# Kernel tuning notes

Hardware: AMD Instinct MI355X
Metric: run time of the kernel (lower is better)

## Reference

```python
import jax, jax.numpy as jnp
import numpy as np

N, IN_DIM, OUT_DIM, H = 50000, 128, 128, 4
C = OUT_DIM // H  # 32, per-head channels
E = 1_600_000
NEG_SLOPE = 0.2
LN_EPS = 1e-5


def setup_inputs() -> dict:
    key = jax.random.key(0)
    ks = jax.random.split(key, 12)
    x = jax.random.normal(ks[0], (N, IN_DIM), dtype=jnp.float32)
    edge_index = jax.random.randint(ks[1], (2, E), 0, N, dtype=jnp.int64)
    edge_weight = jax.random.uniform(ks[2], (E,), dtype=jnp.float32)
    s = 1.0 / np.sqrt(IN_DIM)
    W = jax.random.normal(ks[3], (IN_DIM, H * C), dtype=jnp.float32) * s
    att_src = jax.random.normal(ks[4], (1, H, C), dtype=jnp.float32) * s
    att_dst = jax.random.normal(ks[5], (1, H, C), dtype=jnp.float32) * s
    W_edge = jax.random.normal(ks[6], (1, H * C), dtype=jnp.float32)
    att_edge = jax.random.normal(ks[7], (1, H, C), dtype=jnp.float32) * s
    bias = jnp.zeros((H * C,), dtype=jnp.float32)
    ln_gamma = jnp.ones((OUT_DIM,), dtype=jnp.float32)
    ln_beta = jnp.zeros((OUT_DIM,), dtype=jnp.float32)
    return {"x": x, "edge_index": edge_index, "edge_weight": edge_weight,
            "W": W, "att_src": att_src, "att_dst": att_dst,
            "W_edge": W_edge, "att_edge": att_edge, "bias": bias,
            "ln_gamma": ln_gamma, "ln_beta": ln_beta}


def _gat_forward(x, edge_index, edge_weight, W, att_src, att_dst, W_edge, att_edge, bias):
    # GATConv(in, C, heads=H, edge_dim=1), concat=True, add_self_loops=True (fill_value='mean')
    xp = (x @ W).reshape(N, H, C)                      # [N,H,C]
    a_src = jnp.sum(xp * att_src, axis=-1)             # [N,H]
    a_dst = jnp.sum(xp * att_dst, axis=-1)             # [N,H]

    # add self-loops; self-loop edge_attr = mean of existing edge_attr
    loop = jnp.arange(N, dtype=edge_index.dtype)
    src = jnp.concatenate([edge_index[0], loop])       # [E+N]
    dst = jnp.concatenate([edge_index[1], loop])
    ew = jnp.concatenate([edge_weight, jnp.full((N,), jnp.mean(edge_weight), edge_weight.dtype)])

    ea = (ew[:, None] @ W_edge).reshape(-1, H, C)      # [E+N,H,C]
    a_edge = jnp.sum(ea * att_edge, axis=-1)           # [E+N,H]

    logits = a_src[src] + a_dst[dst] + a_edge          # [E+N,H]
    logits = jax.nn.leaky_relu(logits, NEG_SLOPE)

    # segment softmax over destination-node neighborhoods
    m = jax.ops.segment_max(logits, dst, num_segments=N)     # [N,H]
    ex = jnp.exp(logits - m[dst])
    denom = jax.ops.segment_sum(ex, dst, num_segments=N)     # [N,H]
    attn = ex / (denom[dst] + 1e-16)                          # [E+N,H]

    msg = attn[:, :, None] * xp[src]                          # [E+N,H,C]
    out = jax.ops.segment_sum(msg, dst, num_segments=N)      # [N,H,C]
    return out.reshape(N, H * C) + bias


def reference(x, edge_index, edge_weight, W, att_src, att_dst, W_edge, att_edge, bias, ln_gamma, ln_beta):
    out = _gat_forward(x, edge_index, edge_weight, W, att_src, att_dst, W_edge, att_edge, bias)
    # LayerNorm
    mu = jnp.mean(out, axis=-1, keepdims=True)
    var = jnp.mean(jnp.square(out - mu), axis=-1, keepdims=True)
    out = (out - mu) / jnp.sqrt(var + LN_EPS) * ln_gamma + ln_beta
    # ELU (dropout is identity in eval)
    return jax.nn.elu(out)
```

## Files before the change

### kernel.cpp

```cpp
#include <hip/hip_runtime.h>
#include <hip/hip_fp16.h>
#include <cstddef>

#define N_NODES 50000
#define E_EDGES 1600000
#define NEG_SLOPE 0.2f
#define LN_EPS 1e-5f
#define LOG2E 1.4426950408889634f
#define PAD 96

#define NBK 196
#define BCAP 10240
#define PCH 4096
#define NCH 391
#define NGB 1563
#define TPB 256

#define OFF_SCAL    0u
#define OFF_BCUR    256u
#define OFF_EWPART  2048u
#define OFF_COUNTS  8192u
#define OFF_ASRC    208256u
#define OFF_ADST    1008256u
#define OFF_XPH     1808256u
#define OFF_PAIRS   14608256u
#define OFF_STAGE   33808256u

__device__ __forceinline__ float lrelu(float x) { return x > 0.f ? x : NEG_SLOPE * x; }

__device__ __forceinline__ float sel4(float4 v, int h) {
    float ab = (h & 1) ? v.y : v.x;
    float cd = (h & 1) ? v.w : v.z;
    return (h & 2) ? cd : ab;
}

__device__ __forceinline__ float4 fma4(float s, float4 a, float4 c) {
    c.x = fmaf(s, a.x, c.x); c.y = fmaf(s, a.y, c.y);
    c.z = fmaf(s, a.z, c.z); c.w = fmaf(s, a.w, c.w);
    return c;
}

__global__ __launch_bounds__(256, 5) void k_A(const float* __restrict__ x, const float* __restrict__ W,
                                              const float* __restrict__ att_src, const float* __restrict__ att_dst,
                                              const float* __restrict__ W_edge, const float* __restrict__ att_edge,
                                              const int* __restrict__ ei, const float* __restrict__ ew,
                                              unsigned short* __restrict__ xph, float* __restrict__ a_src,
                                              float* __restrict__ a_dst, float* __restrict__ scal,
                                              int* __restrict__ bcur, uint2* __restrict__ staging,
                                              float* __restrict__ ewPart) {
    __shared__ float sx[32 * 128];
    __shared__ float sW[32 * 128];
    int t = threadIdx.x;

    if (blockIdx.x < NCH) {
        int* cnt   = (int*)sx;
        int* gbase = cnt + NBK;
        float* wred = (float*)(gbase + NBK);
        for (int i = t; i < NBK; i += 256) cnt[i] = 0;
        __syncthreads();

        int e0 = blockIdx.x * PCH;
        int lr[16];
        float s_ew = 0.f;
        #pragma unroll
        for (int i = 0; i < 16; i++) {
            int e = e0 + i * 256 + t;
            lr[i] = 0;
            if (e < E_EDGES) {
                int d = ei[E_EDGES + e];
                s_ew += ew[e];
                lr[i] = atomicAdd(&cnt[d >> 8], 1);
            }
        }
        #pragma unroll
        for (int off = 32; off; off >>= 1) s_ew += __shfl_down(s_ew, off, 64);
        if ((t & 63) == 0) wred[t >> 6] = s_ew;
        __syncthreads();
        if (t == 0) ewPart[blockIdx.x] = wred[0] + wred[1] + wred[2] + wred[3];
        for (int i = t; i < NBK; i += 256) gbase[i] = atomicAdd(&bcur[i], cnt[i]);
        __syncthreads();

        #pragma unroll
        for (int i = 0; i < 16; i++) {
            int e = e0 + i * 256 + t;
            if (e < E_EDGES) {
                int s = ei[e];
                int d = ei[E_EDGES + e];
                float w = ew[e];
                int b = d >> 8;
                uint2 ent;
                ent.x = (unsigned int)s |
                        ((unsigned int)__half_as_ushort(__float2half_rn(w)) << 16);
                ent.y = (unsigned int)d;
                staging[(size_t)b * BCAP + gbase[b] + lr[i]] = ent;
            }
        }
        return;
    }

    int gb = blockIdx.x - NCH;
    if (gb == 0 && t < 128) {
        float p = W_edge[t] * att_edge[t];
        #pragma unroll
        for (int off = 16; off; off >>= 1) p += __shfl_down(p, off, 32);
        if ((t & 31) == 0) scal[4 + (t >> 5)] = p;
    }
    int r0 = gb * 32;
    int tc = t & 31;
    int tr = t >> 5;

    for (int i = t; i < 1024; i += 256) {
        int row = i >> 5;
        float4 v = make_float4(0.f, 0.f, 0.f, 0.f);
        if (r0 + row < N_NODES) v = ((const float4*)x)[(size_t)(r0 + row) * 32 + (i & 31)];
        ((float4*)sx)[i] = v;
    }

    float4 acc[4];
    #pragma unroll
    for (int r = 0; r < 4; r++) acc[r] = make_float4(0.f, 0.f, 0.f, 0.f);

    for (int kc = 0; kc < 128; kc += 32) {
        __syncthreads();
        for (int i = t; i < 1024; i += 256)
            ((float4*)sW)[i] = ((const float4*)W)[(size_t)kc * 32 + i];
        __syncthreads();
        #pragma unroll 4
        for (int k4 = 0; k4 < 8; k4++) {
            float4 w0 = ((float4*)sW)[(k4 * 4 + 0) * 32 + tc];
            float4 w1 = ((float4*)sW)[(k4 * 4 + 1) * 32 + tc];
            float4 w2 = ((float4*)sW)[(k4 * 4 + 2) * 32 + tc];
            float4 w3 = ((float4*)sW)[(k4 * 4 + 3) * 32 + tc];
            #pragma unroll
            for (int r = 0; r < 4; r++) {
                float4 xv = ((float4*)sx)[(tr * 4 + r) * 32 + (kc >> 2) + k4];
                acc[r] = fma4(xv.x, w0, acc[r]);
                acc[r] = fma4(xv.y, w1, acc[r]);
                acc[r] = fma4(xv.z, w2, acc[r]);
                acc[r] = fma4(xv.w, w3, acc[r]);
            }
        }
    }

    float4 s4 = ((const float4*)att_src)[tc];
    float4 d4 = ((const float4*)att_dst)[tc];
    int h = tc >> 3;
    #pragma unroll
    for (int r = 0; r < 4; r++) {
        int row = r0 + tr * 4 + r;
        if (row < N_NODES) {
            __half2 h01 = __floats2half2_rn(acc[r].x, acc[r].y);
            __half2 h23 = __floats2half2_rn(acc[r].z, acc[r].w);
            uint2 pk;
            pk.x = *(unsigned int*)&h01;
            pk.y = *(unsigned int*)&h23;
            ((uint2*)xph)[(size_t)row * 32 + tc] = pk;
            float ps = acc[r].x * s4.x + acc[r].y * s4.y + acc[r].z * s4.z + acc[r].w * s4.w;
            float pd = acc[r].x * d4.x + acc[r].y * d4.y + acc[r].z * d4.z + acc[r].w * d4.w;
            ps += __shfl_down(ps, 4, 8); ps += __shfl_down(ps, 2, 8); ps += __shfl_down(ps, 1, 8);
            pd += __shfl_down(pd, 4, 8); pd += __shfl_down(pd, 2, 8); pd += __shfl_down(pd, 1, 8);
            if ((tc & 7) == 0) {
                a_src[(size_t)row * 4 + h] = ps;
                a_dst[(size_t)row * 4 + h] = pd;
            }
        }
    }
}

__global__ __launch_bounds__(256) void k_p2(const uint2* __restrict__ staging,
                                            const int* __restrict__ bcur,
                                            const float* __restrict__ ewPart,
                                            unsigned int* __restrict__ pairs,
                                            int* __restrict__ counts, float* __restrict__ scal) {
    int b = blockIdx.x, t = threadIdx.x;
    __shared__ int cnt2[256];
    __shared__ float wr2[4];
    if (b == 0) {
        float s = 0.f;
        for (int i = t; i < NCH; i += 256) s += ewPart[i];
        #pragma unroll
        for (int off = 32; off; off >>= 1) s += __shfl_down(s, off, 64);
        if ((t & 63) == 0) wr2[t >> 6] = s;
    }
    cnt2[t] = 0;
    __syncthreads();
    if (b == 0 && t == 0) scal[0] = wr2[0] + wr2[1] + wr2[2] + wr2[3];
    int tot = bcur[b];
    const uint2* sg = staging + (size_t)b * BCAP;
    for (int i = t; i < tot; i += 256) {
        uint2 ent = sg[i];
        int d = (int)ent.y;
        int r = atomicAdd(&cnt2[d & 255], 1);
        pairs[(size_t)d * PAD + r] = ent.x;
    }
    __syncthreads();
    int n = (b << 8) + t;
    if (n < N_NODES) counts[n] = cnt2[t];
}

__global__ __launch_bounds__(256) void k_p3(const unsigned int* __restrict__ xpu,
                                            const float* __restrict__ a_src,
                                            const float* __restrict__ a_dst,
                                            const int* __restrict__ counts,
                                            const unsigned int* __restrict__ pairs,
                                            const float* __restrict__ scal,
                                            const float* __restrict__ bias,
                                            const float* __restrict__ gamma,
                                            const float* __restrict__ beta,
                                            float* __restrict__ out) {
    __shared__ unsigned long long sal[4][4][100];
    int lane = threadIdx.x & 63;
    int wv = threadIdx.x >> 6;
    int n = blockIdx.x * 4 + wv;
    if (n >= N_NODES) return;

    int h = lane >> 4;
    int em = lane & 15;

    float4 K = *(const float4*)(scal + 4);
    float Kh = sel4(K, h);
    float mean_ew = scal[0] * (1.0f / E_EDGES);

    int cnt = __builtin_amdgcn_readfirstlane(counts[n]);
    float4 ad4 = *(const float4*)(a_dst + (size_t)4 * n);
    float4 as4 = *(const float4*)(a_src + (size_t)4 * n);
    float adh = sel4(ad4, h);
    float aself = exp2f(lrelu(sel4(as4, h) + adh + Kh * mean_ew) * LOG2E);

    unsigned int pv = xpu[(size_t)n * 64 + lane];
    float2 f = __half22float2(*(__half2*)&pv);
    float acc0 = aself * f.x, acc1 = aself * f.y;

    unsigned long long* sl = &sal[wv][h][0];
    const unsigned int* prow = pairs + (size_t)n * PAD;
    float den = 0.f;
    #pragma unroll
    for (int b = 0; b < 6; b++) {
        if (b * 16 < cnt) {
            int e = b * 16 + em;
            float alpha = 0.f;
            int s = n;
            if (e < cnt) {
                unsigned int pk = prow[e];
                s = (int)(pk & 0xFFFFu);
                float w = __half2float(__ushort_as_half((unsigned short)(pk >> 16)));
                float4 av = *(const float4*)(a_src + (size_t)4 * s);
                alpha = exp2f(lrelu(sel4(av, h) + adh + Kh * w) * LOG2E);
            }
            den += alpha;
            sl[e] = ((unsigned long long)__float_as_uint(alpha) << 32) | (unsigned int)s;
        }
    }

    int cnt4 = (cnt + 3) & ~3;
    for (int e = 0; e < cnt4; e += 4) {
        ulonglong2 p01 = *(const ulonglong2*)(sl + e);
        ulonglong2 p23 = *(const ulonglong2*)(sl + e + 2);
        unsigned long long pq[4] = {p01.x, p01.y, p23.x, p23.y};
        #pragma unroll
        for (int q = 0; q < 4; q++) {
            unsigned int sj = (unsigned int)pq[q];
            float aj = __uint_as_float((unsigned int)(pq[q] >> 32));
            unsigned int g = xpu[(size_t)sj * 64 + lane];
            __half2 hh = *(__half2*)&g;
            acc0 = fmaf(aj, __half2float(__low2half(hh)), acc0);
            acc1 = fmaf(aj, __half2float(__high2half(hh)), acc1);
        }
    }

    den += __shfl_xor(den, 1, 64);
    den += __shfl_xor(den, 2, 64);
    den += __shfl_xor(den, 4, 64);
    den += __shfl_xor(den, 8, 64);
    den += aself;

    float inv = 1.0f / (den + 1e-16f);
    float2 b2 = ((const float2*)bias)[lane];
    float y0 = fmaf(acc0, inv, b2.x);
    float y1 = fmaf(acc1, inv, b2.y);

    float s1 = y0 + y1;
    #pragma unroll
    for (int off = 1; off < 64; off <<= 1) s1 += __shfl_xor(s1, off, 64);
    float mu = s1 * (1.f / 128.f);
    float d0 = y0 - mu, d1 = y1 - mu;
    float s2 = d0 * d0 + d1 * d1;
    #pragma unroll
    for (int off = 1; off < 64; off <<= 1) s2 += __shfl_xor(s2, off, 64);
    float rstd = rsqrtf(s2 * (1.f / 128.f) + LN_EPS);
    float2 g2 = ((const float2*)gamma)[lane];
    float2 be2 = ((const float2*)beta)[lane];
    float o0 = fmaf(d0 * rstd, g2.x, be2.x);
    float o1 = fmaf(d1 * rstd, g2.y, be2.y);
    o0 = o0 > 0.f ? o0 : expm1f(o0);
    o1 = o1 > 0.f ? o1 : expm1f(o1);
    float2 o; o.x = o0; o.y = o1;
    ((float2*)out)[(size_t)n * 64 + lane] = o;
}

extern "C" void kernel_launch(void* const* d_in, const int* in_sizes, int n_in,
                              void* d_out, int out_size, void* d_ws, size_t ws_size,
                              hipStream_t stream) {
    const float* x        = (const float*)d_in[0];
    const int*   ei       = (const int*)d_in[1];
    const float* ew       = (const float*)d_in[2];
    const float* W        = (const float*)d_in[3];
    const float* att_src  = (const float*)d_in[4];
    const float* att_dst  = (const float*)d_in[5];
    const float* W_edge   = (const float*)d_in[6];
    const float* att_edge = (const float*)d_in[7];
    const float* bias     = (const float*)d_in[8];
    const float* gamma    = (const float*)d_in[9];
    const float* beta     = (const float*)d_in[10];
    float* out = (float*)d_out;

    char* ws = (char*)d_ws;
    float* scal      = (float*)(ws + OFF_SCAL);
    int*   bcur      = (int*)(ws + OFF_BCUR);
    float* ewPart    = (float*)(ws + OFF_EWPART);
    int*   counts    = (int*)(ws + OFF_COUNTS);
    float* a_src     = (float*)(ws + OFF_ASRC);
    float* a_dst     = (float*)(ws + OFF_ADST);
    unsigned short* xph = (unsigned short*)(ws + OFF_XPH);
    unsigned int* pairs = (unsigned int*)(ws + OFF_PAIRS);
    uint2* staging   = (uint2*)(ws + OFF_STAGE);

    hipMemsetAsync(bcur, 0, NBK * sizeof(int), stream);
    k_A<<<NCH + NGB, TPB, 0, stream>>>(x, W, att_src, att_dst, W_edge, att_edge, ei, ew,
                                       xph, a_src, a_dst, scal, bcur, staging, ewPart);
    k_p2<<<NBK, TPB, 0, stream>>>(staging, bcur, ewPart, pairs, counts, scal);
    k_p3<<<12500, TPB, 0, stream>>>((const unsigned int*)xph, a_src, a_dst, counts, pairs, scal,
                                    bias, gamma, beta, out);
}
```

Baseline: 217.3 us.

## Replace two-pass bucketed edge scatter with direct global-atomic CSR build

Removes the staging buffer and the separate k_p2 bucket-redistribution kernel. Each edge now takes a slot with a global atomicAdd on counts[dst] and writes its packed (src, half weight) entry straight into the padded pairs array. The edge-weight sum is accumulated with one global float atomic per block instead of per-block partials. This cuts one kernel launch and a round trip of staging traffic, but adds 1.6M global atomics on random addresses, scattered 4-byte writes, and a larger memset.

```diff
diff --git a/kernel.cpp b/kernel.cpp
--- a/kernel.cpp
+++ b/kernel.cpp
@@ -9,22 +9,18 @@
 #define LOG2E 1.4426950408889634f
 #define PAD 96
 
-#define NBK 196
-#define BCAP 10240
 #define PCH 4096
 #define NCH 391
 #define NGB 1563
 #define TPB 256
 
 #define OFF_SCAL    0u
-#define OFF_BCUR    256u
-#define OFF_EWPART  2048u
 #define OFF_COUNTS  8192u
 #define OFF_ASRC    208256u
 #define OFF_ADST    1008256u
 #define OFF_XPH     1808256u
 #define OFF_PAIRS   14608256u
-#define OFF_STAGE   33808256u
+#define MEMSET_BYTES 208192u
 
 __device__ __forceinline__ float lrelu(float x) { return x > 0.f ? x : NEG_SLOPE * x; }
 
@@ -46,40 +42,14 @@
                                               const int* __restrict__ ei, const float* __restrict__ ew,
                                               unsigned short* __restrict__ xph, float* __restrict__ a_src,
                                               float* __restrict__ a_dst, float* __restrict__ scal,
-                                              int* __restrict__ bcur, uint2* __restrict__ staging,
-                                              float* __restrict__ ewPart) {
+                                              int* __restrict__ counts, unsigned int* __restrict__ pairs) {
     __shared__ float sx[32 * 128];
     __shared__ float sW[32 * 128];
     int t = threadIdx.x;
 
     if (blockIdx.x < NCH) {
-        int* cnt   = (int*)sx;
-        int* gbase = cnt + NBK;
-        float* wred = (float*)(gbase + NBK);
-        for (int i = t; i < NBK; i += 256) cnt[i] = 0;
-        __syncthreads();
-
         int e0 = blockIdx.x * PCH;
-        int lr[16];
         float s_ew = 0.f;
-        #pragma unroll
-        for (int i = 0; i < 16; i++) {
-            int e = e0 + i * 256 + t;
-            lr[i] = 0;
-            if (e < E_EDGES) {
-                int d = ei[E_EDGES + e];
-                s_ew += ew[e];
-                lr[i] = atomicAdd(&cnt[d >> 8], 1);
-            }
-        }
-        #pragma unroll
-        for (int off = 32; off; off >>= 1) s_ew += __shfl_down(s_ew, off, 64);
-        if ((t & 63) == 0) wred[t >> 6] = s_ew;
-        __syncthreads();
-        if (t == 0) ewPart[blockIdx.x] = wred[0] + wred[1] + wred[2] + wred[3];
-        for (int i = t; i < NBK; i += 256) gbase[i] = atomicAdd(&bcur[i], cnt[i]);
-        __syncthreads();
-
         #pragma unroll
         for (int i = 0; i < 16; i++) {
             int e = e0 + i * 256 + t;
@@ -87,14 +57,19 @@
                 int s = ei[e];
                 int d = ei[E_EDGES + e];
                 float w = ew[e];
-                int b = d >> 8;
-                uint2 ent;
-                ent.x = (unsigned int)s |
-                        ((unsigned int)__half_as_ushort(__float2half_rn(w)) << 16);
-                ent.y = (unsigned int)d;
-                staging[(size_t)b * BCAP + gbase[b] + lr[i]] = ent;
-            }
-        }
+                s_ew += w;
+                int r = atomicAdd(&counts[d], 1);
+                unsigned int pk = (unsigned int)s |
+                                  ((unsigned int)__half_as_ushort(__float2half_rn(w)) << 16);
+                pairs[(size_t)d * PAD + r] = pk;
+            }
+        }
+        #pragma unroll
+        for (int off = 32; off; off >>= 1) s_ew += __shfl_down(s_ew, off, 64);
+        float* wred = (float*)sx;
+        if ((t & 63) == 0) wred[t >> 6] = s_ew;
+        __syncthreads();
+        if (t == 0) atomicAdd(scal, wred[0] + wred[1] + wred[2] + wred[3]);
         return;
     }
 
@@ -167,37 +142,6 @@
     }
 }
 
-__global__ __launch_bounds__(256) void k_p2(const uint2* __restrict__ staging,
-                                            const int* __restrict__ bcur,
-                                            const float* __restrict__ ewPart,
-                                            unsigned int* __restrict__ pairs,
-                                            int* __restrict__ counts, float* __restrict__ scal) {
-    int b = blockIdx.x, t = threadIdx.x;
-    __shared__ int cnt2[256];
-    __shared__ float wr2[4];
-    if (b == 0) {
-        float s = 0.f;
-        for (int i = t; i < NCH; i += 256) s += ewPart[i];
-        #pragma unroll
-        for (int off = 32; off; off >>= 1) s += __shfl_down(s, off, 64);
-        if ((t & 63) == 0) wr2[t >> 6] = s;
-    }
-    cnt2[t] = 0;
-    __syncthreads();
-    if (b == 0 && t == 0) scal[0] = wr2[0] + wr2[1] + wr2[2] + wr2[3];
-    int tot = bcur[b];
-    const uint2* sg = staging + (size_t)b * BCAP;
-    for (int i = t; i < tot; i += 256) {
-        uint2 ent = sg[i];
-        int d = (int)ent.y;
-        int r = atomicAdd(&cnt2[d & 255], 1);
-        pairs[(size_t)d * PAD + r] = ent.x;
-    }
-    __syncthreads();
-    int n = (b << 8) + t;
-    if (n < N_NODES) counts[n] = cnt2[t];
-}
-
 __global__ __launch_bounds__(256) void k_p3(const unsigned int* __restrict__ xpu,
                                             const float* __restrict__ a_src,
                                             const float* __restrict__ a_dst,
@@ -316,19 +260,15 @@
 
     char* ws = (char*)d_ws;
     float* scal      = (float*)(ws + OFF_SCAL);
-    int*   bcur      = (int*)(ws + OFF_BCUR);
-    float* ewPart    = (float*)(ws + OFF_EWPART);
     int*   counts    = (int*)(ws + OFF_COUNTS);
     float* a_src     = (float*)(ws + OFF_ASRC);
     float* a_dst     = (float*)(ws + OFF_ADST);
     unsigned short* xph = (unsigned short*)(ws + OFF_XPH);
     unsigned int* pairs = (unsigned int*)(ws + OFF_PAIRS);
-    uint2* staging   = (uint2*)(ws + OFF_STAGE);
-
-    hipMemsetAsync(bcur, 0, NBK * sizeof(int), stream);
+
+    hipMemsetAsync(ws, 0, MEMSET_BYTES, stream);
     k_A<<<NCH + NGB, TPB, 0, stream>>>(x, W, att_src, att_dst, W_edge, att_edge, ei, ew,
-                                       xph, a_src, a_dst, scal, bcur, staging, ewPart);
-    k_p2<<<NBK, TPB, 0, stream>>>(staging, bcur, ewPart, pairs, counts, scal);
+                                       xph, a_src, a_dst, scal, counts, pairs);
     k_p3<<<12500, TPB, 0, stream>>>((const unsigned int*)xph, a_src, a_dst, counts, pairs, scal,
                                     bias, gamma, beta, out);
 }
```

Measured after the change: 269.8 us. 24.2% more time.
